# Kernel optimization log

Measured on AMD Instinct MI355X. Metric: run time of the kernel, lower is better.

Reference implementation:

```python
import jax, jax.numpy as jnp
import numpy as np

N = 500_000
IN_FEAT = 128
HIDDEN = 128
OUT_FEAT = 128
CODE_DIM = 32
NUM_CODES = 256


def _linear_params(key, fan_in, fan_out):
    kw, kb = jax.random.split(key)
    bound = 1.0 / np.sqrt(fan_in)
    W = jax.random.uniform(kw, (fan_out, fan_in), jnp.float32, -bound, bound)
    b = jax.random.uniform(kb, (fan_out,), jnp.float32, -bound, bound)
    return W, b


def setup_inputs() -> dict:
    key = jax.random.key(0)
    ks = jax.random.split(key, 6)
    x = jax.random.normal(ks[0], (N, IN_FEAT), jnp.float32)
    W_down, b_down = _linear_params(ks[1], IN_FEAT, HIDDEN)
    W_pin, b_pin = _linear_params(ks[2], HIDDEN, CODE_DIM)      # VQ project_in 128->32
    codebook = jax.random.normal(ks[3], (NUM_CODES, CODE_DIM), jnp.float32)
    W_pout, b_pout = _linear_params(ks[4], CODE_DIM, HIDDEN)    # VQ project_out 32->128
    W_up, b_up = _linear_params(ks[5], HIDDEN, OUT_FEAT)
    return {"x": x, "W_down": W_down, "b_down": b_down,
            "W_pin": W_pin, "b_pin": b_pin, "codebook": codebook,
            "W_pout": W_pout, "b_pout": b_pout,
            "W_up": W_up, "b_up": b_up}


def reference(x, W_down, b_down, W_pin, b_pin, codebook, W_pout, b_pout, W_up, b_up):
    # down: Linear(128 -> 128)
    h = x @ W_down.T + b_down                                   # [N, 128]
    # VQ project_in: Linear(128 -> 32)
    z = h @ W_pin.T + b_pin                                     # [N, 32]
    # squared euclidean distance to codebook, argmin assignment
    d2 = (jnp.sum(z * z, axis=-1, keepdims=True)
          - 2.0 * (z @ codebook.T)
          + jnp.sum(codebook * codebook, axis=-1))              # [N, 256]
    indices = jnp.argmin(d2, axis=-1)                           # [N] int
    q = codebook[indices]                                       # gather [N, 32]
    # straight-through estimator
    q_ste = z + jax.lax.stop_gradient(q - z)
    # VQ project_out: Linear(32 -> 128)
    v = q_ste @ W_pout.T + b_pout                               # [N, 128]
    # up: Linear(128 -> 128), then clamp
    y = jnp.clip(v @ W_up.T + b_up, -1.0, 1.0)                  # [N, 128]
    # commitment_weight = 0 -> commit loss is exactly zero
    commit_loss = jnp.zeros((), x.dtype)
    return y, indices, commit_loss
```

## Files before the change

kernel.cpp:

```cpp
#include <hip/hip_runtime.h>


#define CODE_D 32
#define NUM_C  256
#define KCH    32
#define LSTR   36


__global__ void vq_prep1(const float* __restrict__ Wd, const float* __restrict__ bd,
                         const float* __restrict__ Wp, const float* __restrict__ bp,
                         const float* __restrict__ cb,
                         float* __restrict__ Wc, float* __restrict__ bc,
                         float* __restrict__ cbias) {
    const int t = threadIdx.x;
    for (int e = t; e < 32 * 128; e += 256) {
        const int j = e >> 7, k = e & 127;
        double s = 0.0;
        for (int m = 0; m < 128; ++m)
            s += (double)Wp[j * 128 + m] * (double)Wd[m * 128 + k];
        Wc[e] = (float)s;
    }
    if (t < 32) {
        double s = (double)bp[t];
        for (int m = 0; m < 128; ++m) s += (double)Wp[t * 128 + m] * (double)bd[m];
        bc[t] = (float)s;
    }
    {
        float s = 0.f;
        for (int d = 0; d < CODE_D; ++d) { float v = cb[t * CODE_D + d]; s += v * v; }
        cbias[t] = -0.5f * s;
    }
}

__global__ void vq_prep2(const float* __restrict__ cb, const float* __restrict__ Wpo,
                         const float* __restrict__ bpo, const float* __restrict__ Wu,
                         const float* __restrict__ bu, float* __restrict__ ytab) {
    __shared__ float v[128];
    const int c = blockIdx.x;
    const int t = threadIdx.x;
    float s = bpo[t];
    for (int d = 0; d < CODE_D; ++d) s += cb[c * CODE_D + d] * Wpo[t * CODE_D + d];
    v[t] = s;
    __syncthreads();
    float o = bu[t];
    for (int m = 0; m < 128; ++m) o += v[m] * Wu[t * 128 + m];
    o = fminf(fmaxf(o, -1.0f), 1.0f);
    ytab[c * 128 + t] = o;
}


__global__ __launch_bounds__(256, 4) void vq_main(
    const float* __restrict__ x,
    const float* __restrict__ Wc,
    const float* __restrict__ bc,
    const float* __restrict__ cb,
    const float* __restrict__ cbias,
    const float* __restrict__ ytab,
    float* __restrict__ y,
    float* __restrict__ idx_out,
    float* __restrict__ loss_out,
    int N) {
    __shared__ float lds[256 * LSTR];
    __shared__ int sidx[256];

    const int t = threadIdx.x;
    const int row0 = blockIdx.x * 256;
    const int myrow = row0 + t;

    float z[CODE_D];
#pragma unroll
    for (int j = 0; j < CODE_D; ++j) z[j] = bc[j];

    const int rr = t >> 3;
    const int qq = t & 7;
    for (int kc = 0; kc < 128; kc += KCH) {
#pragma unroll
        for (int i = 0; i < 8; ++i) {
            const int r = i * 32 + rr;
            const int grow = row0 + r;
            float4 v = make_float4(0.f, 0.f, 0.f, 0.f);
            if (grow < N)
                v = *reinterpret_cast<const float4*>(x + (size_t)grow * 128 + kc + qq * 4);
            *reinterpret_cast<float4*>(&lds[r * LSTR + qq * 4]) = v;
        }
        __syncthreads();
#pragma unroll
        for (int q = 0; q < KCH / 4; ++q) {
            const float4 xv = *reinterpret_cast<const float4*>(&lds[t * LSTR + q * 4]);
            const int kb = kc + q * 4;
#pragma unroll
            for (int j = 0; j < CODE_D; ++j) {
                const float* w = Wc + j * 128 + kb;
                z[j] += w[0] * xv.x + w[1] * xv.y + w[2] * xv.z + w[3] * xv.w;
            }
        }
        __syncthreads();
    }

    float best = -3.0e38f;
    int besti = 0;
#pragma unroll 4
    for (int c = 0; c < NUM_C; ++c) {
        const float* crow = cb + c * CODE_D;
        float s0 = 0.f, s1 = 0.f, s2 = 0.f, s3 = 0.f;
#pragma unroll
        for (int d = 0; d < CODE_D; d += 4) {
            s0 += crow[d + 0] * z[d + 0];
            s1 += crow[d + 1] * z[d + 1];
            s2 += crow[d + 2] * z[d + 2];
            s3 += crow[d + 3] * z[d + 3];
        }
        const float s = ((s0 + s1) + (s2 + s3)) + cbias[c];
        if (s > best) { best = s; besti = c; }
    }

    sidx[t] = besti;
    if (myrow < N) idx_out[myrow] = (float)besti;
    __syncthreads();

    const int rsub = t >> 5;
    const int c4 = t & 31;
#pragma unroll
    for (int i = 0; i < 32; ++i) {
        const int r = i * 8 + rsub;
        const int grow = row0 + r;
        if (grow < N) {
            const int ci = sidx[r];
            const float4 v = *reinterpret_cast<const float4*>(ytab + ci * 128 + c4 * 4);
            *reinterpret_cast<float4*>(y + (size_t)grow * 128 + c4 * 4) = v;
        }
    }

    if (blockIdx.x == 0 && t == 0) loss_out[0] = 0.0f;
}


extern "C" void kernel_launch(void* const* d_in, const int* in_sizes, int n_in,
                              void* d_out, int out_size, void* d_ws, size_t ws_size,
                              hipStream_t stream) {
    const float* x   = (const float*)d_in[0];
    const float* Wd  = (const float*)d_in[1];
    const float* bd  = (const float*)d_in[2];
    const float* Wp  = (const float*)d_in[3];
    const float* bp  = (const float*)d_in[4];
    const float* cb  = (const float*)d_in[5];
    const float* Wpo = (const float*)d_in[6];
    const float* bpo = (const float*)d_in[7];
    const float* Wu  = (const float*)d_in[8];
    const float* bu  = (const float*)d_in[9];

    const int N = in_sizes[0] / 128;

    float* ws    = (float*)d_ws;
    float* Wc    = ws;
    float* bc    = ws + 4096;
    float* cbias = ws + 4128;
    float* ytab  = ws + 4384;

    float* y    = (float*)d_out;
    float* idxf = y + (size_t)N * 128;
    float* loss = idxf + N;

    vq_prep1<<<1, 256, 0, stream>>>(Wd, bd, Wp, bp, cb, Wc, bc, cbias);
    vq_prep2<<<NUM_C, 128, 0, stream>>>(cb, Wpo, bpo, Wu, bu, ytab);

    const int blocks = (N + 255) / 256;
    vq_main<<<blocks, 256, 0, stream>>>(x, Wc, bc, cb, cbias, ytab, y, idxf, loss, N);
}
```

Before: 933.9 us.

## Process two rows per thread, stage codebook in LDS, parallelize prep kernel

Each thread now handles two rows, so every codebook element loaded is reused for two distance computations. The codebook and its bias are staged in shared memory rather than read from global memory. The single-block prep kernel is split across 17 blocks to shorten the serial setup. The costs are more registers per thread (launch bounds lowered to 2 blocks per CU), extra LDS use, and half as many blocks in flight.

```diff
diff --git a/kernel.cpp b/kernel.cpp
--- a/kernel.cpp
+++ b/kernel.cpp
@@ -13,19 +13,20 @@
                          float* __restrict__ Wc, float* __restrict__ bc,
                          float* __restrict__ cbias) {
     const int t = threadIdx.x;
-    for (int e = t; e < 32 * 128; e += 256) {
+    const int b = blockIdx.x;
+    if (b < 16) {
+        const int e = b * 256 + t;
         const int j = e >> 7, k = e & 127;
         double s = 0.0;
         for (int m = 0; m < 128; ++m)
             s += (double)Wp[j * 128 + m] * (double)Wd[m * 128 + k];
         Wc[e] = (float)s;
-    }
-    if (t < 32) {
-        double s = (double)bp[t];
-        for (int m = 0; m < 128; ++m) s += (double)Wp[t * 128 + m] * (double)bd[m];
-        bc[t] = (float)s;
-    }
-    {
+    } else {
+        if (t < 32) {
+            double s = (double)bp[t];
+            for (int m = 0; m < 128; ++m) s += (double)Wp[t * 128 + m] * (double)bd[m];
+            bc[t] = (float)s;
+        }
         float s = 0.f;
         for (int d = 0; d < CODE_D; ++d) { float v = cb[t * CODE_D + d]; s += v * v; }
         cbias[t] = -0.5f * s;
@@ -49,7 +50,7 @@
 }
 
 
-__global__ __launch_bounds__(256, 4) void vq_main(
+__global__ __launch_bounds__(256, 2) void vq_main(
     const float* __restrict__ x,
     const float* __restrict__ Wc,
     const float* __restrict__ bc,
@@ -60,74 +61,99 @@
     float* __restrict__ idx_out,
     float* __restrict__ loss_out,
     int N) {
-    __shared__ float lds[256 * LSTR];
-    __shared__ int sidx[256];
+    __shared__ float xs[256 * LSTR];
+    __shared__ float cbs[NUM_C * CODE_D];
+    __shared__ float cbb[NUM_C];
+    __shared__ int   sidx[512];
 
     const int t = threadIdx.x;
-    const int row0 = blockIdx.x * 256;
-    const int myrow = row0 + t;
+    const int row0 = blockIdx.x * 512;
 
-    float z[CODE_D];
+    {
+        const float4* src = (const float4*)cb;
+        float4* dst = (float4*)cbs;
 #pragma unroll
-    for (int j = 0; j < CODE_D; ++j) z[j] = bc[j];
+        for (int i = 0; i < 8; ++i) dst[t + i * 256] = src[t + i * 256];
+        cbb[t] = cbias[t];
+    }
+
+    float z[2][CODE_D];
+#pragma unroll
+    for (int j = 0; j < CODE_D; ++j) { const float b = bc[j]; z[0][j] = b; z[1][j] = b; }
 
     const int rr = t >> 3;
     const int qq = t & 7;
-    for (int kc = 0; kc < 128; kc += KCH) {
 #pragma unroll
-        for (int i = 0; i < 8; ++i) {
-            const int r = i * 32 + rr;
-            const int grow = row0 + r;
-            float4 v = make_float4(0.f, 0.f, 0.f, 0.f);
-            if (grow < N)
-                v = *reinterpret_cast<const float4*>(x + (size_t)grow * 128 + kc + qq * 4);
-            *reinterpret_cast<float4*>(&lds[r * LSTR + qq * 4]) = v;
-        }
-        __syncthreads();
+    for (int h = 0; h < 2; ++h) {
+        const int rb = row0 + h * 256;
+        for (int kc = 0; kc < 128; kc += KCH) {
+            __syncthreads();
 #pragma unroll
-        for (int q = 0; q < KCH / 4; ++q) {
-            const float4 xv = *reinterpret_cast<const float4*>(&lds[t * LSTR + q * 4]);
-            const int kb = kc + q * 4;
+            for (int i = 0; i < 8; ++i) {
+                const int r = i * 32 + rr;
+                const int g = rb + r;
+                float4 v = make_float4(0.f, 0.f, 0.f, 0.f);
+                if (g < N)
+                    v = *reinterpret_cast<const float4*>(x + (size_t)g * 128 + kc + qq * 4);
+                *reinterpret_cast<float4*>(&xs[r * LSTR + qq * 4]) = v;
+            }
+            __syncthreads();
 #pragma unroll
-            for (int j = 0; j < CODE_D; ++j) {
-                const float* w = Wc + j * 128 + kb;
-                z[j] += w[0] * xv.x + w[1] * xv.y + w[2] * xv.z + w[3] * xv.w;
+            for (int q = 0; q < KCH / 4; ++q) {
+                const float4 xv = *reinterpret_cast<const float4*>(&xs[t * LSTR + q * 4]);
+                const int kb = kc + q * 4;
+#pragma unroll
+                for (int j = 0; j < CODE_D; ++j) {
+                    const float* w = Wc + j * 128 + kb;
+                    z[h][j] += w[0] * xv.x + w[1] * xv.y + w[2] * xv.z + w[3] * xv.w;
+                }
             }
         }
-        __syncthreads();
     }
 
-    float best = -3.0e38f;
-    int besti = 0;
-#pragma unroll 4
+    float bestA = -3.0e38f, bestB = -3.0e38f;
+    int biA = 0, biB = 0;
+#pragma unroll 2
     for (int c = 0; c < NUM_C; ++c) {
-        const float* crow = cb + c * CODE_D;
-        float s0 = 0.f, s1 = 0.f, s2 = 0.f, s3 = 0.f;
+        const float* crow = cbs + c * CODE_D;
+        float sA0 = 0.f, sA1 = 0.f, sA2 = 0.f, sA3 = 0.f;
+        float sB0 = 0.f, sB1 = 0.f, sB2 = 0.f, sB3 = 0.f;
 #pragma unroll
         for (int d = 0; d < CODE_D; d += 4) {
-            s0 += crow[d + 0] * z[d + 0];
-            s1 += crow[d + 1] * z[d + 1];
-            s2 += crow[d + 2] * z[d + 2];
-            s3 += crow[d + 3] * z[d + 3];
+            const float c0 = crow[d + 0], c1 = crow[d + 1];
+            const float c2 = crow[d + 2], c3 = crow[d + 3];
+            sA0 += c0 * z[0][d + 0];
+            sA1 += c1 * z[0][d + 1];
+            sA2 += c2 * z[0][d + 2];
+            sA3 += c3 * z[0][d + 3];
+            sB0 += c0 * z[1][d + 0];
+            sB1 += c1 * z[1][d + 1];
+            sB2 += c2 * z[1][d + 2];
+            sB3 += c3 * z[1][d + 3];
         }
-        const float s = ((s0 + s1) + (s2 + s3)) + cbias[c];
-        if (s > best) { best = s; besti = c; }
+        const float bias = cbb[c];
+        const float sA = ((sA0 + sA1) + (sA2 + sA3)) + bias;
+        const float sB = ((sB0 + sB1) + (sB2 + sB3)) + bias;
+        if (sA > bestA) { bestA = sA; biA = c; }
+        if (sB > bestB) { bestB = sB; biB = c; }
     }
 
-    sidx[t] = besti;
-    if (myrow < N) idx_out[myrow] = (float)besti;
+    sidx[t] = biA;
+    sidx[t + 256] = biB;
+    if (row0 + t < N) idx_out[row0 + t] = (float)biA;
+    if (row0 + 256 + t < N) idx_out[row0 + 256 + t] = (float)biB;
     __syncthreads();
 
     const int rsub = t >> 5;
     const int c4 = t & 31;
-#pragma unroll
-    for (int i = 0; i < 32; ++i) {
+#pragma unroll 4
+    for (int i = 0; i < 64; ++i) {
         const int r = i * 8 + rsub;
-        const int grow = row0 + r;
-        if (grow < N) {
+        const int g = row0 + r;
+        if (g < N) {
             const int ci = sidx[r];
             const float4 v = *reinterpret_cast<const float4*>(ytab + ci * 128 + c4 * 4);
-            *reinterpret_cast<float4*>(y + (size_t)grow * 128 + c4 * 4) = v;
+            *reinterpret_cast<float4*>(y + (size_t)g * 128 + c4 * 4) = v;
         }
     }
 
@@ -161,9 +187,9 @@
     float* idxf = y + (size_t)N * 128;
     float* loss = idxf + N;
 
-    vq_prep1<<<1, 256, 0, stream>>>(Wd, bd, Wp, bp, cb, Wc, bc, cbias);
+    vq_prep1<<<17, 256, 0, stream>>>(Wd, bd, Wp, bp, cb, Wc, bc, cbias);
     vq_prep2<<<NUM_C, 128, 0, stream>>>(cb, Wpo, bpo, Wu, bu, ytab);
 
-    const int blocks = (N + 255) / 256;
+    const int blocks = (N + 511) / 512;
     vq_main<<<blocks, 256, 0, stream>>>(x, Wc, bc, cb, cbias, ytab, y, idxf, loss, N);
 }
```

Measured after the change: 1.156 ms. 1.24x slower.
